# Optimization experiments

Hardware: AMD Instinct MI355X
Metric: run time of the kernel (lower is better)

The kernel has to match this reference:

```python
import jax, jax.numpy as jnp
import numpy as np

NUM_HEADS = 16
DIM_PER_HEAD = 64
DIM = 1024
B, L = 2, 2048
SCALE = DIM_PER_HEAD ** -0.5


def setup_inputs() -> dict:
    key = jax.random.key(0)
    k1, k2, k3, k4, k5 = jax.random.split(key, 5)
    inner = NUM_HEADS * DIM_PER_HEAD
    x = jax.random.normal(k1, (B, L, DIM), dtype=jnp.float32)
    mask = jax.random.randint(k2, (B, L, L), 0, 2, dtype=jnp.int32)
    W_qkv = jax.random.normal(k3, (DIM, 3 * inner), dtype=jnp.float32) * (DIM ** -0.5)
    W_out = jax.random.normal(k4, (inner, DIM), dtype=jnp.float32) * (inner ** -0.5)
    b_out = jax.random.normal(k5, (DIM,), dtype=jnp.float32) * 0.01
    return {"x": x, "mask": mask, "W_qkv": W_qkv, "W_out": W_out, "b_out": b_out}


def reference(x, mask, W_qkv, W_out, b_out):
    b, l, _ = x.shape
    h, d = NUM_HEADS, DIM_PER_HEAD
    # qkv: [b, l, 3, h, d] -> q/k/v each [b, h, l, d]
    qkv = (x @ W_qkv).reshape(b, l, 3, h, d)
    qkv = jnp.transpose(qkv, (2, 0, 3, 1, 4))
    q, k, v = qkv[0], qkv[1], qkv[2]
    scores = jnp.einsum('bhid,bhjd->bhij', q, k) * SCALE
    attn = jax.nn.softmax(scores, axis=-1)
    # post-softmax mask multiply + renormalize (matches original)
    m = mask[:, None, :, :].astype(attn.dtype)
    attn = attn * m
    attn = attn / (attn.sum(axis=-1, keepdims=True) + 1e-10)
    z = jnp.einsum('bhij,bhjd->bhid', attn, v)
    z = jnp.transpose(z, (0, 2, 1, 3)).reshape(b, l, h * d)
    return z @ W_out + b_out
```

## Files before the change

kernel.cpp:

```cpp
#include <hip/hip_runtime.h>

typedef __attribute__((ext_vector_type(8))) short bf16x8;
typedef __attribute__((ext_vector_type(4))) float f32x4;
typedef __attribute__((ext_vector_type(4))) unsigned short us4;
typedef __attribute__((ext_vector_type(4))) unsigned int u32x4;
typedef unsigned short us;

#define SCALE 0.125f

__device__ __forceinline__ unsigned short f2bf(float f) {
    unsigned int u = __float_as_uint(f);
    u = (u + 0x7FFF + ((u >> 16) & 1)) >> 16;
    return (unsigned short)u;
}


__global__ __launch_bounds__(256) void convx(const float* __restrict__ X,
                                             unsigned short* __restrict__ O) {
    int i = blockIdx.x * 256 + threadIdx.x;
    float4 v = ((const float4*)X)[i];
    us4 o;
    o.x = f2bf(v.x); o.y = f2bf(v.y); o.z = f2bf(v.z); o.w = f2bf(v.w);
    ((us4*)O)[i] = o;
}

__global__ __launch_bounds__(256) void transposew(const float* __restrict__ W,
                                                  unsigned short* __restrict__ WT,
                                                  int Kd, int Cd) {
    __shared__ float t[32][33];
    int c0 = blockIdx.x * 32, k0 = blockIdx.y * 32;
    int tx = threadIdx.x & 31, ty = threadIdx.x >> 5;
#pragma unroll
    for (int i = 0; i < 32; i += 8)
        t[ty + i][tx] = W[(size_t)(k0 + ty + i) * Cd + c0 + tx];
    __syncthreads();
#pragma unroll
    for (int i = 0; i < 32; i += 8)
        WT[(size_t)(c0 + ty + i) * Kd + k0 + tx] = f2bf(t[tx][ty + i]);
}

__global__ __launch_bounds__(256) void packmask(const int* __restrict__ Mi,
                                                unsigned int* __restrict__ Mo) {
    int i = blockIdx.x * 256 + threadIdx.x;
    int4 v = ((const int4*)Mi)[i];
    Mo[i] = (unsigned)(v.x & 1) | ((unsigned)(v.y & 1) << 8) |
            ((unsigned)(v.z & 1) << 16) | ((unsigned)(v.w & 1) << 24);
}

template <int MODE>
__global__ __launch_bounds__(256) void gemm_bf16(
    const unsigned short* __restrict__ A, const unsigned short* __restrict__ BT,
    int M, int N, int K,
    unsigned short* __restrict__ Qo, unsigned short* __restrict__ Ko,
    unsigned short* __restrict__ Vo,
    const float* __restrict__ bias, float* __restrict__ Co) {
    __shared__ unsigned short Asub[128 * 64];
    __shared__ unsigned short Bsub[128 * 64];
    const int bm = blockIdx.y, bn = blockIdx.x;
    const int tid = threadIdx.x, w = tid >> 6, lane = tid & 63;
    const int wr = w >> 1, wc = w & 1, l16 = lane & 15, lg = lane >> 4;

    f32x4 acc[4][4];
#pragma unroll
    for (int i = 0; i < 4; i++)
#pragma unroll
        for (int j = 0; j < 4; j++) acc[i][j] = (f32x4){0.f, 0.f, 0.f, 0.f};

    const int r_st = tid >> 3;
    const int kc_st = (tid & 7) * 8;

    const int nkt = K / 64;
    for (int kt = 0; kt < nkt; kt++) {
        const int k0 = kt * 64;
#pragma unroll
        for (int i = 0; i < 4; i++) {
            int r = r_st + i * 32;
            uint4 va = *(const uint4*)(A + (size_t)(bm * 128 + r) * K + k0 + kc_st);
            uint4 vb = *(const uint4*)(BT + (size_t)(bn * 128 + r) * K + k0 + kc_st);
            int byt = (r * 128 + kc_st * 2) ^ ((r & 7) << 4);
            *(uint4*)((char*)Asub + byt) = va;
            *(uint4*)((char*)Bsub + byt) = vb;
        }
        __syncthreads();
#pragma unroll
        for (int ks = 0; ks < 2; ks++) {
            bf16x8 af[4], bfr[4];
            int kk = ks * 32 + lg * 8;
#pragma unroll
            for (int i = 0; i < 4; i++) {
                int r = wr * 64 + i * 16 + l16;
                af[i] = *(bf16x8*)((char*)Asub + ((r * 128 + kk * 2) ^ ((r & 7) << 4)));
                int c = wc * 64 + i * 16 + l16;
                bfr[i] = *(bf16x8*)((char*)Bsub + ((c * 128 + kk * 2) ^ ((c & 7) << 4)));
            }
#pragma unroll
            for (int i = 0; i < 4; i++)
#pragma unroll
                for (int j = 0; j < 4; j++)
                    acc[i][j] = __builtin_amdgcn_mfma_f32_16x16x32_bf16(
                        af[i], bfr[j], acc[i][j], 0, 0, 0);
        }
        __syncthreads();
    }

    if (MODE == 0) {
#pragma unroll
        for (int i = 0; i < 4; i++) {
            int grow = bm * 128 + wr * 64 + i * 16 + lg * 4;
            int bb = grow >> 11, ll = grow & 2047;
#pragma unroll
            for (int j = 0; j < 4; j++) {
                int gcol = bn * 128 + wc * 64 + j * 16 + l16;
                int s = gcol >> 10, hh = (gcol >> 6) & 15, dd = gcol & 63;
                int bhh = bb * 16 + hh;
                if (s == 2) {
                    us4 pk;
                    pk.x = f2bf(acc[i][j][0]); pk.y = f2bf(acc[i][j][1]);
                    pk.z = f2bf(acc[i][j][2]); pk.w = f2bf(acc[i][j][3]);
                    *(us4*)(Vo + (size_t)(bhh * 64 + dd) * 2048 + ll) = pk;
                } else {
                    unsigned short* dst =
                        (s == 0 ? Qo : Ko) + (size_t)(bhh * 2048 + ll) * 64 + dd;
#pragma unroll
                    for (int r = 0; r < 4; r++) dst[(size_t)r * 64] = f2bf(acc[i][j][r]);
                }
            }
        }
    } else {
#pragma unroll
        for (int i = 0; i < 4; i++) {
            int grow = bm * 128 + wr * 64 + i * 16 + lg * 4;
#pragma unroll
            for (int j = 0; j < 4; j++) {
                int gcol = bn * 128 + wc * 64 + j * 16 + l16;
                float bv = bias[gcol];
#pragma unroll
                for (int r = 0; r < 4; r++)
                    Co[(size_t)(grow + r) * N + gcol] = acc[i][j][r] + bv;
            }
        }
    }
}

__global__ __launch_bounds__(256, 4) void flash_attn(
    const us* __restrict__ Q, const us* __restrict__ Kt,
    const us* __restrict__ VT, const unsigned char* __restrict__ M8,
    us* __restrict__ Z) {
    __shared__ char lds[2][20480];
    const int bh = blockIdx.y;
    const int b = bh >> 4, h = bh & 15;
    const int tid = threadIdx.x, w = tid >> 6, lane = tid & 63;
    const int l16 = lane & 15, lg = lane >> 4;
    const int qb0 = blockIdx.x * 64;
    const int qrow = qb0 + w * 16 + l16;

    const size_t kbh = (size_t)bh * 2048;
    const size_t vbh = (size_t)bh * 64;

    const us* Qp = Q + (size_t)(kbh + qrow) * 64 + lg * 8;
    bf16x8 qf0 = *(const bf16x8*)(Qp);
    bf16x8 qf1 = *(const bf16x8*)(Qp + 32);

    float m_r = -__builtin_inff();
    float l_r = 0.f;
    f32x4 oacc[4];
#pragma unroll
    for (int jd = 0; jd < 4; jd++) oacc[jd] = (f32x4){0.f, 0.f, 0.f, 0.f};

    const int L0 = l16 + (((2 * lg) & 3) << 4);
    const int L1 = l16 + (((2 * lg + 1) & 3) << 4);
    const bool hi = (lg >> 1) != 0;

    int koff[8], voff[8], moff[4];
#pragma unroll
    for (int j = 0; j < 4; j++)
#pragma unroll
        for (int hh = 0; hh < 2; hh++)
            koff[2 * j + hh] = (16 * j + l16) * 128 + ((64 * hh + 16 * lg) ^ ((l16 & 7) << 4));
#pragma unroll
    for (int ks = 0; ks < 2; ks++)
#pragma unroll
        for (int jd = 0; jd < 4; jd++)
            voff[ks * 4 + jd] =
                8192 + (jd * 16 + l16) * 128 + ((64 * ks + 16 * lg) ^ ((l16 & 7) << 4));
#pragma unroll
    for (int j = 0; j < 4; j++)
        moff[j] = 16384 + (w * 16 + l16) * 64 + ((16 * j + 4 * lg) ^ ((l16 & 3) << 4));

    const int wbase = (tid & ~63) * 16;

    auto STAGE = [&](int bufi, int kt) {
        char* base = &lds[bufi][0];
        const int lk = kt * 64;
#pragma unroll
        for (int i = 0; i < 2; i++) {
            int slot = i * 256 + tid;
            int r = slot >> 3, blk = slot & 7;
            const us* src = Kt + (kbh + lk + r) * 64 + ((blk ^ (r & 7)) << 3);
            __builtin_amdgcn_global_load_lds(
                (const __attribute__((address_space(1))) unsigned*)src,
                (__attribute__((address_space(3))) unsigned*)(base + i * 4096 + wbase),
                16, 0, 0);
        }
#pragma unroll
        for (int i = 0; i < 2; i++) {
            int slot = i * 256 + tid;
            int r = slot >> 3, blk = slot & 7;
            const us* src = VT + (vbh + r) * 2048 + lk + ((blk ^ (r & 7)) << 3);
            __builtin_amdgcn_global_load_lds(
                (const __attribute__((address_space(1))) unsigned*)src,
                (__attribute__((address_space(3))) unsigned*)(base + 8192 + i * 4096 + wbase),
                16, 0, 0);
        }
        {
            int r = tid >> 2, mb = tid & 3;
            const unsigned char* src =
                M8 + (size_t)(b * 2048 + qb0 + r) * 2048 + lk + ((mb ^ (r & 3)) << 4);
            __builtin_amdgcn_global_load_lds(
                (const __attribute__((address_space(1))) unsigned*)src,
                (__attribute__((address_space(3))) unsigned*)(base + 16384 + wbase),
                16, 0, 0);
        }
    };

    STAGE(0, 0);
    asm volatile("s_waitcnt vmcnt(0) lgkmcnt(0)" ::: "memory");
    __builtin_amdgcn_sched_barrier(0);
    __syncthreads();
    int cur = 0;

    for (int kt = 0; kt < 32; kt++) {
        if (kt < 31) STAGE(cur ^ 1, kt + 1);
        char* Lb = &lds[cur][0];
        unsigned mw[4];
#pragma unroll
        for (int j = 0; j < 4; j++) mw[j] = *(const unsigned*)(Lb + moff[j]);
        bf16x8 kf[8];
#pragma unroll
        for (int q8 = 0; q8 < 8; q8++) kf[q8] = *(const bf16x8*)(Lb + koff[q8]);
        f32x4 sacc[4];
#pragma unroll
        for (int j = 0; j < 4; j++) sacc[j] = (f32x4){0.f, 0.f, 0.f, 0.f};
#pragma unroll
        for (int j = 0; j < 4; j++) {
            sacc[j] = __builtin_amdgcn_mfma_f32_16x16x32_bf16(kf[2 * j], qf0, sacc[j], 0, 0, 0);
            sacc[j] = __builtin_amdgcn_mfma_f32_16x16x32_bf16(kf[2 * j + 1], qf1, sacc[j], 0, 0, 0);
        }
        float ss[4][4];
#pragma unroll
        for (int j = 0; j < 4; j++)
#pragma unroll
            for (int r = 0; r < 4; r++) ss[j][r] = sacc[j][r] * SCALE;
        float mx0 = fmaxf(fmaxf(ss[0][0], ss[0][1]), fmaxf(ss[0][2], ss[0][3]));
        float mx1 = fmaxf(fmaxf(ss[1][0], ss[1][1]), fmaxf(ss[1][2], ss[1][3]));
        float mx2 = fmaxf(fmaxf(ss[2][0], ss[2][1]), fmaxf(ss[2][2], ss[2][3]));
        float mx3 = fmaxf(fmaxf(ss[3][0], ss[3][1]), fmaxf(ss[3][2], ss[3][3]));
        float mx = fmaxf(fmaxf(mx0, mx1), fmaxf(mx2, mx3));
        mx = fmaxf(mx, __shfl_xor(mx, 16));
        mx = fmaxf(mx, __shfl_xor(mx, 32));
        float mn = fmaxf(m_r, mx);
        float alpha = __expf(m_r - mn);
        m_r = mn;
        unsigned W[4][2];
        float rs = 0.f;
#pragma unroll
        for (int j = 0; j < 4; j++) {
            uchar4 mu = __builtin_bit_cast(uchar4, mw[j]);
            float p0 = __expf(ss[j][0] - mn) * (float)mu.x;
            float p1 = __expf(ss[j][1] - mn) * (float)mu.y;
            float p2 = __expf(ss[j][2] - mn) * (float)mu.z;
            float p3 = __expf(ss[j][3] - mn) * (float)mu.w;
            rs += (p0 + p1) + (p2 + p3);
            W[j][0] = __builtin_amdgcn_perm(__float_as_uint(p1), __float_as_uint(p0),
                                            0x07060302u);
            W[j][1] = __builtin_amdgcn_perm(__float_as_uint(p3), __float_as_uint(p2),
                                            0x07060302u);
        }
        rs += __shfl_xor(rs, 16);
        rs += __shfl_xor(rs, 32);
        l_r = l_r * alpha + rs;
#pragma unroll
        for (int jd = 0; jd < 4; jd++) {
            oacc[jd][0] *= alpha; oacc[jd][1] *= alpha;
            oacc[jd][2] *= alpha; oacc[jd][3] *= alpha;
        }
#pragma unroll
        for (int ks = 0; ks < 2; ks++) {
            bf16x8 vf[4];
#pragma unroll
            for (int jd = 0; jd < 4; jd++)
                vf[jd] = *(const bf16x8*)(Lb + voff[ks * 4 + jd]);
            unsigned a0 = __shfl((int)W[2 * ks][0], L0), b0 = __shfl((int)W[2 * ks + 1][0], L0);
            unsigned a1 = __shfl((int)W[2 * ks][1], L0), b1 = __shfl((int)W[2 * ks + 1][1], L0);
            unsigned a2 = __shfl((int)W[2 * ks][0], L1), b2 = __shfl((int)W[2 * ks + 1][0], L1);
            unsigned a3 = __shfl((int)W[2 * ks][1], L1), b3 = __shfl((int)W[2 * ks + 1][1], L1);
            u32x4 pw = (u32x4){hi ? b0 : a0, hi ? b1 : a1, hi ? b2 : a2, hi ? b3 : a3};
            bf16x8 pB = __builtin_bit_cast(bf16x8, pw);
#pragma unroll
            for (int jd = 0; jd < 4; jd++)
                oacc[jd] = __builtin_amdgcn_mfma_f32_16x16x32_bf16(vf[jd], pB,
                                                                   oacc[jd], 0, 0, 0);
        }
        asm volatile("s_waitcnt vmcnt(0) lgkmcnt(0)" ::: "memory");
        __builtin_amdgcn_sched_barrier(0);
        __syncthreads();
        cur ^= 1;
    }

    const float inv = 1.0f / (l_r + 1e-20f);
    us* zp = Z + (size_t)(b * 2048 + qrow) * 1024 + h * 64 + lg * 4;
#pragma unroll
    for (int jd = 0; jd < 4; jd++) {
        us4 pk;
        pk.x = f2bf(oacc[jd][0] * inv);
        pk.y = f2bf(oacc[jd][1] * inv);
        pk.z = f2bf(oacc[jd][2] * inv);
        pk.w = f2bf(oacc[jd][3] * inv);
        *(us4*)(zp + jd * 16) = pk;
    }
}


extern "C" void kernel_launch(void* const* d_in, const int* in_sizes, int n_in,
                              void* d_out, int out_size, void* d_ws, size_t ws_size,
                              hipStream_t stream) {
    const float* x = (const float*)d_in[0];
    const int* mask = (const int*)d_in[1];
    const float* Wqkv = (const float*)d_in[2];
    const float* Wout = (const float*)d_in[3];
    const float* bout = (const float*)d_in[4];
    float* out = (float*)d_out;
    char* ws = (char*)d_ws;

    unsigned short* xz    = (unsigned short*)(ws);
    unsigned short* wqkvT = (unsigned short*)(ws + (8u << 20));
    unsigned short* woutT = (unsigned short*)(ws + (14u << 20));
    unsigned char*  m8    = (unsigned char*)(ws + (16u << 20));
    unsigned short* Qb    = (unsigned short*)(ws + (24u << 20));
    unsigned short* Kb    = (unsigned short*)(ws + (32u << 20));
    unsigned short* VTb   = (unsigned short*)(ws + (40u << 20));

    convx<<<4096, 256, 0, stream>>>(x, xz);
    transposew<<<dim3(3072 / 32, 1024 / 32), 256, 0, stream>>>(Wqkv, wqkvT, 1024, 3072);
    transposew<<<dim3(1024 / 32, 1024 / 32), 256, 0, stream>>>(Wout, woutT, 1024, 1024);
    packmask<<<8192, 256, 0, stream>>>(mask, (unsigned int*)m8);
    gemm_bf16<0><<<dim3(3072 / 128, 4096 / 128), 256, 0, stream>>>(
        xz, wqkvT, 4096, 3072, 1024, Qb, Kb, VTb, nullptr, nullptr);
    flash_attn<<<dim3(32, 32), 256, 0, stream>>>(Qb, Kb, VTb, m8, xz);
    gemm_bf16<1><<<dim3(1024 / 128, 4096 / 128), 256, 0, stream>>>(
        xz, woutT, 4096, 1024, 1024, nullptr, nullptr, nullptr, bout, out);
}
```

Measured before the change: 178.6 us.

## Fold softmax scale into Q, use exp2 with lazy rescale, and async LDS loads in GEMM

The QKV GEMM epilogue now pre-multiplies Q by scale*log2(e), so the attention loop can drop its per-score scaling and use the native exp2. The running max is only updated when the new max exceeds the old by more than a threshold, which skips most alpha rescales of the accumulators. The GEMM tile loads now use global_load_lds direct-to-LDS transfers with an XOR swizzle applied on the source address instead of register staging. The lazy rescale lets probabilities grow up to 2^8 before rescaling, which adds some bf16/fp32 range risk.

```diff
diff --git a/kernel.cpp b/kernel.cpp
--- a/kernel.cpp
+++ b/kernel.cpp
@@ -6,7 +6,7 @@
 typedef __attribute__((ext_vector_type(4))) unsigned int u32x4;
 typedef unsigned short us;
 
-#define SCALE 0.125f
+#define C2 0.18033688011112042f
 
 __device__ __forceinline__ unsigned short f2bf(float f) {
     unsigned int u = __float_as_uint(f);
@@ -66,21 +66,28 @@
 #pragma unroll
         for (int j = 0; j < 4; j++) acc[i][j] = (f32x4){0.f, 0.f, 0.f, 0.f};
 
-    const int r_st = tid >> 3;
-    const int kc_st = (tid & 7) * 8;
+    const int wbase = (tid & ~63) * 16;
 
     const int nkt = K / 64;
     for (int kt = 0; kt < nkt; kt++) {
         const int k0 = kt * 64;
 #pragma unroll
         for (int i = 0; i < 4; i++) {
-            int r = r_st + i * 32;
-            uint4 va = *(const uint4*)(A + (size_t)(bm * 128 + r) * K + k0 + kc_st);
-            uint4 vb = *(const uint4*)(BT + (size_t)(bn * 128 + r) * K + k0 + kc_st);
-            int byt = (r * 128 + kc_st * 2) ^ ((r & 7) << 4);
-            *(uint4*)((char*)Asub + byt) = va;
-            *(uint4*)((char*)Bsub + byt) = vb;
-        }
+            int slot = i * 256 + tid;
+            int r = slot >> 3, blk = slot & 7;
+            const us* srcA = A + (size_t)(bm * 128 + r) * K + k0 + ((blk ^ (r & 7)) << 3);
+            __builtin_amdgcn_global_load_lds(
+                (const __attribute__((address_space(1))) unsigned*)srcA,
+                (__attribute__((address_space(3))) unsigned*)((char*)Asub + i * 4096 + wbase),
+                16, 0, 0);
+            const us* srcB = BT + (size_t)(bn * 128 + r) * K + k0 + ((blk ^ (r & 7)) << 3);
+            __builtin_amdgcn_global_load_lds(
+                (const __attribute__((address_space(1))) unsigned*)srcB,
+                (__attribute__((address_space(3))) unsigned*)((char*)Bsub + i * 4096 + wbase),
+                16, 0, 0);
+        }
+        asm volatile("s_waitcnt vmcnt(0)" ::: "memory");
+        __builtin_amdgcn_sched_barrier(0);
         __syncthreads();
 #pragma unroll
         for (int ks = 0; ks < 2; ks++) {
@@ -118,9 +125,13 @@
                     pk.x = f2bf(acc[i][j][0]); pk.y = f2bf(acc[i][j][1]);
                     pk.z = f2bf(acc[i][j][2]); pk.w = f2bf(acc[i][j][3]);
                     *(us4*)(Vo + (size_t)(bhh * 64 + dd) * 2048 + ll) = pk;
+                } else if (s == 0) {
+                    unsigned short* dst = Qo + (size_t)(bhh * 2048 + ll) * 64 + dd;
+#pragma unroll
+                    for (int r = 0; r < 4; r++)
+                        dst[(size_t)r * 64] = f2bf(acc[i][j][r] * C2);
                 } else {
-                    unsigned short* dst =
-                        (s == 0 ? Qo : Ko) + (size_t)(bhh * 2048 + ll) * 64 + dd;
+                    unsigned short* dst = Ko + (size_t)(bhh * 2048 + ll) * 64 + dd;
 #pragma unroll
                     for (int r = 0; r < 4; r++) dst[(size_t)r * 64] = f2bf(acc[i][j][r]);
                 }
@@ -246,30 +257,32 @@
             sacc[j] = __builtin_amdgcn_mfma_f32_16x16x32_bf16(kf[2 * j], qf0, sacc[j], 0, 0, 0);
             sacc[j] = __builtin_amdgcn_mfma_f32_16x16x32_bf16(kf[2 * j + 1], qf1, sacc[j], 0, 0, 0);
         }
-        float ss[4][4];
-#pragma unroll
-        for (int j = 0; j < 4; j++)
-#pragma unroll
-            for (int r = 0; r < 4; r++) ss[j][r] = sacc[j][r] * SCALE;
-        float mx0 = fmaxf(fmaxf(ss[0][0], ss[0][1]), fmaxf(ss[0][2], ss[0][3]));
-        float mx1 = fmaxf(fmaxf(ss[1][0], ss[1][1]), fmaxf(ss[1][2], ss[1][3]));
-        float mx2 = fmaxf(fmaxf(ss[2][0], ss[2][1]), fmaxf(ss[2][2], ss[2][3]));
-        float mx3 = fmaxf(fmaxf(ss[3][0], ss[3][1]), fmaxf(ss[3][2], ss[3][3]));
+        float mx0 = fmaxf(fmaxf(sacc[0][0], sacc[0][1]), fmaxf(sacc[0][2], sacc[0][3]));
+        float mx1 = fmaxf(fmaxf(sacc[1][0], sacc[1][1]), fmaxf(sacc[1][2], sacc[1][3]));
+        float mx2 = fmaxf(fmaxf(sacc[2][0], sacc[2][1]), fmaxf(sacc[2][2], sacc[2][3]));
+        float mx3 = fmaxf(fmaxf(sacc[3][0], sacc[3][1]), fmaxf(sacc[3][2], sacc[3][3]));
         float mx = fmaxf(fmaxf(mx0, mx1), fmaxf(mx2, mx3));
         mx = fmaxf(mx, __shfl_xor(mx, 16));
         mx = fmaxf(mx, __shfl_xor(mx, 32));
-        float mn = fmaxf(m_r, mx);
-        float alpha = __expf(m_r - mn);
-        m_r = mn;
+        if (mx > m_r + 8.f) {
+            float alpha = __builtin_amdgcn_exp2f(m_r - mx);
+            m_r = mx;
+            l_r *= alpha;
+#pragma unroll
+            for (int jd = 0; jd < 4; jd++) {
+                oacc[jd][0] *= alpha; oacc[jd][1] *= alpha;
+                oacc[jd][2] *= alpha; oacc[jd][3] *= alpha;
+            }
+        }
         unsigned W[4][2];
         float rs = 0.f;
 #pragma unroll
         for (int j = 0; j < 4; j++) {
             uchar4 mu = __builtin_bit_cast(uchar4, mw[j]);
-            float p0 = __expf(ss[j][0] - mn) * (float)mu.x;
-            float p1 = __expf(ss[j][1] - mn) * (float)mu.y;
-            float p2 = __expf(ss[j][2] - mn) * (float)mu.z;
-            float p3 = __expf(ss[j][3] - mn) * (float)mu.w;
+            float p0 = __builtin_amdgcn_exp2f(sacc[j][0] - m_r) * (float)mu.x;
+            float p1 = __builtin_amdgcn_exp2f(sacc[j][1] - m_r) * (float)mu.y;
+            float p2 = __builtin_amdgcn_exp2f(sacc[j][2] - m_r) * (float)mu.z;
+            float p3 = __builtin_amdgcn_exp2f(sacc[j][3] - m_r) * (float)mu.w;
             rs += (p0 + p1) + (p2 + p3);
             W[j][0] = __builtin_amdgcn_perm(__float_as_uint(p1), __float_as_uint(p0),
                                             0x07060302u);
@@ -278,12 +291,7 @@
         }
         rs += __shfl_xor(rs, 16);
         rs += __shfl_xor(rs, 32);
-        l_r = l_r * alpha + rs;
-#pragma unroll
-        for (int jd = 0; jd < 4; jd++) {
-            oacc[jd][0] *= alpha; oacc[jd][1] *= alpha;
-            oacc[jd][2] *= alpha; oacc[jd][3] *= alpha;
-        }
+        l_r += rs;
 #pragma unroll
         for (int ks = 0; ks < 2; ks++) {
             bf16x8 vf[4];
```

Result: no change. 175.8 us (-1.5%).
